# Kernel optimization log

Hardware: AMD Instinct MI355X
Metric: run time of the kernel (lower is better)

The kernel has to match this reference:

```python
import jax, jax.numpy as jnp
import numpy as np

DIM = 256
NUM_HEADS = 8
B = 4
N = 2048
HEAD_DIM = DIM // NUM_HEADS
SCALE = HEAD_DIM ** -0.5
MASK_NEG = -1000.0  # module uses -1000, not -inf


def _block_mask(n):
    # top-left [n/2, n/2] visible, top-right zeroed; bottom [n/2, n] lower-tri with diagonal offset n/2
    half = n // 2
    top = jnp.concatenate([jnp.ones((half, half)), jnp.zeros((half, half))], axis=1)
    bot = jnp.tril(jnp.ones((half, n)), k=half)
    m = jnp.concatenate([top, bot], axis=0)  # [n, n]
    return jnp.where(m != 0, 0.0, MASK_NEG).astype(jnp.float32)


def setup_inputs() -> dict:
    key = jax.random.key(0)
    k1, k2 = jax.random.split(key, 2)
    x = jax.random.normal(k1, (B, N, DIM), dtype=jnp.float32)
    # fused QKV projection params: Linear(dim, 3*dim, bias=True)
    W_qkv = jax.random.normal(k2, (DIM, 3 * DIM), dtype=jnp.float32) * (DIM ** -0.5)
    b_qkv = jnp.zeros((3 * DIM,), dtype=jnp.float32)
    return {"x": x, "W_qkv": W_qkv, "b_qkv": b_qkv}


def reference(x, W_qkv, b_qkv):
    B_, Nn, C = x.shape
    qkv = x @ W_qkv + b_qkv                                   # [B, N, 3C]
    qkv = qkv.reshape(B_, Nn, 3, NUM_HEADS, C // NUM_HEADS)
    qkv = jnp.transpose(qkv, (2, 0, 3, 1, 4))                 # [3, B, H, N, hd]
    q, k, v = qkv[0] * SCALE, qkv[1], qkv[2]
    attn = jnp.einsum('bhqd,bhkd->bhqk', q, k) + _block_mask(Nn)  # [B, H, N, N]
    attn = jax.nn.softmax(attn, axis=-1)
    out = jnp.einsum('bhqk,bhkd->bhqd', attn, v)              # [B, H, N, hd]
    return jnp.transpose(out, (0, 2, 1, 3)).reshape(B_, Nn, C)
```

## Files before the change

kernel.cpp:

```cpp
#include <hip/hip_runtime.h>
#include <cstdint>
#include <cstddef>

typedef unsigned short u16;
typedef unsigned int u32;
typedef __attribute__((ext_vector_type(8))) __bf16 bf16x8;
typedef __attribute__((ext_vector_type(8))) u16 u16x8;
typedef __attribute__((ext_vector_type(4))) float f32x4;

#define N_SEQ   2048
#define HDIM    32
#define QSCALE_LOG2E 0.2550540261150831f

#if __has_builtin(__builtin_amdgcn_exp2f)
#define EXP2(x) __builtin_amdgcn_exp2f(x)
#else
#define EXP2(x) exp2f(x)
#endif

__device__ __forceinline__ u16 f2bf(float f){
  union { float f; u32 i; } v; v.f = f;
  return (u16)((v.i + 0x7FFFu + ((v.i >> 16) & 1u)) >> 16);
}
__device__ __forceinline__ u32 fbits(float f){
  union { float f; u32 i; } v; v.f = f; return v.i;
}
__device__ __forceinline__ u32 pk2bf(float a, float b){
  return ((fbits(a) + 0x8000u) >> 16) | ((fbits(b) + 0x8000u) & 0xFFFF0000u);
}
__device__ __forceinline__ f32x4 mfma_bf16(bf16x8 a, bf16x8 b, f32x4 c){
  return __builtin_amdgcn_mfma_f32_16x16x32_bf16(a, b, c, 0, 0, 0);
}
union U8 { u16x8 u; bf16x8 b; };
union U2 { u32 w[2]; uint64_t q; };

__global__ __launch_bounds__(256) void wt_kernel(const float* __restrict__ W,
                                                 u16* __restrict__ Wt){
  __shared__ u16 T[32][33];
  int t  = threadIdx.x;
  int tx = t & 31, ty = t >> 5;
  int n0 = blockIdx.x * 32;
  int k0 = blockIdx.y * 32;
#pragma unroll
  for (int i = 0; i < 4; ++i){
    int kk = ty + i*8;
    T[kk][tx] = f2bf(W[(k0+kk)*768 + n0 + tx]);
  }
  __syncthreads();
#pragma unroll
  for (int i = 0; i < 4; ++i){
    int nn = ty + i*8;
    Wt[(n0+nn)*256 + k0 + tx] = T[tx][nn];
  }
}

__global__ __launch_bounds__(256) void qkv_kernel(const float* __restrict__ X,
                                                  const u16* __restrict__ Wt,
                                                  const float* __restrict__ bias,
                                                  u16* __restrict__ Q,
                                                  u16* __restrict__ K,
                                                  u16* __restrict__ Vt){
  __shared__ __align__(16) u16 S[64*68];
  int bid = blockIdx.x;
  int xcd = bid & 7;
  int idx = bid >> 3;
  int mt  = 8*(idx & 15) + xcd;
  int nb  = idx >> 4;
  int tid = threadIdx.x;
  int wave = tid >> 6, lane = tid & 63;
  int l16 = lane & 15, quad = lane >> 4;
  int m0 = mt * 64;
  int mw = m0 + wave * 16;
  int n0 = nb * 64;
  const int three = n0 >> 8;

  const float* xr = X + (mw + l16) * 256 + quad * 8;
  U8 af[8];
#pragma unroll
  for (int k = 0; k < 8; ++k){
    f32x4 lo = *(const f32x4*)(xr + k*32);
    f32x4 hi = *(const f32x4*)(xr + k*32 + 4);
    union { u32 w[4]; u16x8 u; } pk;
    pk.w[0] = pk2bf(lo[0], lo[1]);
    pk.w[1] = pk2bf(lo[2], lo[3]);
    pk.w[2] = pk2bf(hi[0], hi[1]);
    pk.w[3] = pk2bf(hi[2], hi[3]);
    af[k].u = pk.u;
  }

  f32x4 acc[4] = {};
#pragma unroll
  for (int k = 0; k < 8; ++k)
#pragma unroll
    for (int s = 0; s < 4; ++s){
      U8 b; b.u = *(const u16x8*)(Wt + (n0 + s*16 + l16)*256 + k*32 + quad*8);
      acc[s] = mfma_bf16(af[k].b, b.b, acc[s]);
    }

  int b_ = m0 >> 11, nseq0 = m0 & 2047;
  if (three == 2){
#pragma unroll
    for (int s = 0; s < 4; ++s){
      int cl = s*16 + l16;
      float bv = bias[n0 + cl];
      int tok = wave*16 + quad*4;
      U2 pk;
      pk.w[0] = pk2bf(acc[s][0] + bv, acc[s][1] + bv);
      pk.w[1] = pk2bf(acc[s][2] + bv, acc[s][3] + bv);
      *(uint64_t*)(&S[cl*68 + tok]) = pk.q;
    }
    __syncthreads();
#pragma unroll
    for (int i = 0; i < 16; ++i){
      int cl = wave*16 + i;
      int c = n0 + cl;
      int h = (c >> 5) & 7, d = c & 31;
      int bh = b_*8 + h;
      int kb = (nseq0 >> 5) + (lane >> 5);
      int kk = lane & 31;
      Vt[((bh*64 + kb)*32 + d)*32 + kk] = S[cl*68 + lane];
    }
  } else {
    float scl = (three == 0) ? QSCALE_LOG2E : 1.0f;
#pragma unroll
    for (int s = 0; s < 4; ++s){
      int cl = s*16 + l16;
      float bv = bias[n0 + cl];
#pragma unroll
      for (int r = 0; r < 4; ++r)
        S[(wave*16 + quad*4 + r)*68 + cl] = f2bf((acc[s][r] + bv) * scl);
    }
    __syncthreads();
    u16* dst = (three == 0) ? Q : K;
#pragma unroll
    for (int j = 0; j < 2; ++j){
      int unit = tid + j*256;
      int tok = unit & 63;
      int rest = unit >> 6;
      int ph = rest >> 2, chunk = rest & 3;
      int h = ((n0 >> 5) + ph) & 7;
      int bh = b_*8 + h;
      u16x8 v = *(const u16x8*)(&S[tok*68 + ph*32 + chunk*8]);
      *(u16x8*)(&dst[(bh*N_SEQ + nseq0 + tok)*HDIM + chunk*8]) = v;
    }
  }
}

__global__ __launch_bounds__(256, 4) void attn_kernel(const u16* __restrict__ Q,
                                                      const u16* __restrict__ Kg,
                                                      const u16* __restrict__ Vt,
                                                      float* __restrict__ out){
  __shared__ __align__(16) u16 smem[4*2*16*72];
  __shared__ float Lbuf[4][32];
  u16  (*Ps)[2][16][72] = (u16 (*)[2][16][72])smem;
  float (*Obuf)[32][36] = (float (*)[32][36])smem;

  int bid = blockIdx.x;
  int bh = (bid & 7)*4 + ((bid >> 3) & 3);
  int g  = bid >> 5;
  int r0 = g * 32;
  int tid = threadIdx.x, wave = tid >> 6, lane = tid & 63;
  int l16 = lane & 15, quad = lane >> 4;

  const u16* Qb = Q  + bh * (N_SEQ*HDIM);
  const u16* Kb = Kg + bh * (N_SEQ*HDIM);
  const u16* Vb = Vt + bh * (64*32*32);

  const int  T       = (r0 < 1024) ? 16 : ((r0 + 31) >> 6) + 1;
  const bool hasMask = (r0 >= 1024);

  U8 qt[2];
  qt[0].u = *(const u16x8*)(Qb + (r0      + l16)*HDIM + quad*8);
  qt[1].u = *(const u16x8*)(Qb + (r0 + 16 + l16)*HDIM + quad*8);

  U8 onesu;
#pragma unroll
  for (int j = 0; j < 8; ++j) onesu.u[j] = 0x3F80;
  bf16x8 ones = onesu.b;

  f32x4 O[2][2] = {};
  f32x4 L[2] = {};

  for (int t = wave; t < T; t += 4){
    int k0 = t * 64;

    U8 kf[4];
#pragma unroll
    for (int s = 0; s < 4; ++s)
      kf[s].u = *(const u16x8*)(Kb + (k0 + s*16 + l16)*HDIM + quad*8);
    U8 vf[2][2];
#pragma unroll
    for (int kc = 0; kc < 2; ++kc)
#pragma unroll
      for (int nd = 0; nd < 2; ++nd)
        vf[kc][nd].u = *(const u16x8*)(Vb + (size_t)(t*2 + kc)*1024 + (nd*16 + l16)*32 + quad*8);

    bool mask = hasMask && (t == T - 1);

#pragma unroll
    for (int qg = 0; qg < 2; ++qg){
      f32x4 ST[4];
#pragma unroll
      for (int s = 0; s < 4; ++s){
        f32x4 z = {};
        ST[s] = mfma_bf16(kf[s].b, qt[qg].b, z);
      }
      u16 (*P)[72] = Ps[wave][qg];
      if (mask){
        int iq = r0 + qg*16 + l16;
#pragma unroll
        for (int s = 0; s < 4; ++s){
          int jb = k0 + s*16 + quad*4;
          float p0 = (jb+0 > iq) ? 0.0f : EXP2(ST[s][0]);
          float p1 = (jb+1 > iq) ? 0.0f : EXP2(ST[s][1]);
          float p2 = (jb+2 > iq) ? 0.0f : EXP2(ST[s][2]);
          float p3 = (jb+3 > iq) ? 0.0f : EXP2(ST[s][3]);
          U2 pk; pk.w[0] = pk2bf(p0, p1); pk.w[1] = pk2bf(p2, p3);
          *(uint64_t*)(&P[l16][s*16 + quad*4]) = pk.q;
        }
      } else {
#pragma unroll
        for (int s = 0; s < 4; ++s){
          U2 pk;
          pk.w[0] = pk2bf(EXP2(ST[s][0]), EXP2(ST[s][1]));
          pk.w[1] = pk2bf(EXP2(ST[s][2]), EXP2(ST[s][3]));
          *(uint64_t*)(&P[l16][s*16 + quad*4]) = pk.q;
        }
      }
    }

#pragma unroll
    for (int qg = 0; qg < 2; ++qg){
      u16 (*P)[72] = Ps[wave][qg];
#pragma unroll
      for (int kc = 0; kc < 2; ++kc){
        U8 pf; pf.u = *(const u16x8*)(&P[l16][kc*32 + quad*8]);
        O[qg][0] = mfma_bf16(pf.b, vf[kc][0].b, O[qg][0]);
        O[qg][1] = mfma_bf16(pf.b, vf[kc][1].b, O[qg][1]);
        L[qg]    = mfma_bf16(pf.b, ones, L[qg]);
      }
    }
  }

  __syncthreads();

#pragma unroll
  for (int qg = 0; qg < 2; ++qg)
#pragma unroll
    for (int r = 0; r < 4; ++r){
      int row = qg*16 + quad*4 + r;
      Obuf[wave][row][l16]      = O[qg][0][r];
      Obuf[wave][row][16 + l16] = O[qg][1][r];
    }
  if (l16 == 0){
#pragma unroll
    for (int qg = 0; qg < 2; ++qg)
#pragma unroll
      for (int r = 0; r < 4; ++r)
        Lbuf[wave][qg*16 + quad*4 + r] = L[qg][r];
  }
  __syncthreads();

  {
    int row = tid >> 3;
    int c4  = (tid & 7) * 4;
    f32x4 a = *(const f32x4*)(&Obuf[0][row][c4]);
    float Ls = Lbuf[0][row];
#pragma unroll
    for (int w = 1; w < 4; ++w){
      f32x4 b = *(const f32x4*)(&Obuf[w][row][c4]);
      a[0] += b[0]; a[1] += b[1]; a[2] += b[2]; a[3] += b[3];
      Ls += Lbuf[w][row];
    }
    float inv = 1.0f / Ls;
    a[0] *= inv; a[1] *= inv; a[2] *= inv; a[3] *= inv;
    int b_ = bh >> 3, h = bh & 7;
    *(f32x4*)(&out[(b_*N_SEQ + r0 + row)*256 + h*32 + c4]) = a;
  }
}

extern "C" void kernel_launch(void* const* d_in, const int* in_sizes, int n_in,
                              void* d_out, int out_size, void* d_ws, size_t ws_size,
                              hipStream_t stream) {
  const float* x    = (const float*)d_in[0];
  const float* W    = (const float*)d_in[1];
  const float* bias = (const float*)d_in[2];
  float* out = (float*)d_out;

  char* ws = (char*)d_ws;
  u16* Wt    = (u16*)(ws);
  u16* Kbuf  = (u16*)(ws + 393216);
  u16* Vtbuf = (u16*)(ws + 393216 + 4194304);
  u16* Qbuf  = (u16*)(ws + 393216 + 2*4194304);

  wt_kernel  <<<dim3(24, 8), 256, 0, stream>>>(W, Wt);
  qkv_kernel <<<dim3(1536),  256, 0, stream>>>(x, Wt, bias, Qbuf, Kbuf, Vtbuf);
  attn_kernel<<<dim3(2048),  256, 0, stream>>>(Qbuf, Kbuf, Vtbuf, out);
}
```

Before: 125.3 us.

## Double attention query tile per block and stage X via LDS with packed W layout

The attention kernel now handles 64 query rows per block instead of 32, with half as many blocks. Each K tile fetched per wave is reused across four query groups, processed in two pairs through the existing P buffer, and the output reduction runs in two passes. The QKV kernel stages the 64x256 X tile into LDS with coalesced loads before building MFMA fragments, and the weight is pre-packed into a fragment-contiguous layout for contiguous B loads. The cost is more registers per attention wave, a larger LDS footprint for the QKV kernel, and fewer blocks to spread across CUs.

```diff
diff --git a/kernel.cpp b/kernel.cpp
--- a/kernel.cpp
+++ b/kernel.cpp
@@ -35,32 +35,27 @@
 union U2 { u32 w[2]; uint64_t q; };
 
 __global__ __launch_bounds__(256) void wt_kernel(const float* __restrict__ W,
-                                                 u16* __restrict__ Wt){
-  __shared__ u16 T[32][33];
+                                                 u16* __restrict__ Wtp){
   int t  = threadIdx.x;
   int tx = t & 31, ty = t >> 5;
   int n0 = blockIdx.x * 32;
   int k0 = blockIdx.y * 32;
 #pragma unroll
   for (int i = 0; i < 4; ++i){
-    int kk = ty + i*8;
-    T[kk][tx] = f2bf(W[(k0+kk)*768 + n0 + tx]);
-  }
-  __syncthreads();
-#pragma unroll
-  for (int i = 0; i < 4; ++i){
-    int nn = ty + i*8;
-    Wt[(n0+nn)*256 + k0 + tx] = T[tx][nn];
+    int k = k0 + ty + i*8;
+    int c = n0 + tx;
+    u16 v = f2bf(W[k*768 + c]);
+    Wtp[((c>>4)*8 + (k>>5))*512 + (c&15)*32 + ((k>>3)&3)*8 + (k&7)] = v;
   }
 }
 
 __global__ __launch_bounds__(256) void qkv_kernel(const float* __restrict__ X,
-                                                  const u16* __restrict__ Wt,
+                                                  const u16* __restrict__ Wtp,
                                                   const float* __restrict__ bias,
                                                   u16* __restrict__ Q,
                                                   u16* __restrict__ K,
                                                   u16* __restrict__ Vt){
-  __shared__ __align__(16) u16 S[64*68];
+  __shared__ __align__(16) u16 SM[64*264];
   int bid = blockIdx.x;
   int xcd = bid & 7;
   int idx = bid >> 3;
@@ -70,30 +65,34 @@
   int wave = tid >> 6, lane = tid & 63;
   int l16 = lane & 15, quad = lane >> 4;
   int m0 = mt * 64;
-  int mw = m0 + wave * 16;
   int n0 = nb * 64;
   const int three = n0 >> 8;
 
-  const float* xr = X + (mw + l16) * 256 + quad * 8;
+  const float* Xblk = X + m0 * 256;
+#pragma unroll
+  for (int i = 0; i < 16; ++i){
+    int e = i*1024 + tid*4;
+    f32x4 v = *(const f32x4*)(Xblk + e);
+    int row = e >> 8, col = e & 255;
+    U2 pk; pk.w[0] = pk2bf(v[0], v[1]); pk.w[1] = pk2bf(v[2], v[3]);
+    *(uint64_t*)(&SM[row*264 + col]) = pk.q;
+  }
+  __syncthreads();
+
+  int mrow = wave*16 + l16;
   U8 af[8];
 #pragma unroll
-  for (int k = 0; k < 8; ++k){
-    f32x4 lo = *(const f32x4*)(xr + k*32);
-    f32x4 hi = *(const f32x4*)(xr + k*32 + 4);
-    union { u32 w[4]; u16x8 u; } pk;
-    pk.w[0] = pk2bf(lo[0], lo[1]);
-    pk.w[1] = pk2bf(lo[2], lo[3]);
-    pk.w[2] = pk2bf(hi[0], hi[1]);
-    pk.w[3] = pk2bf(hi[2], hi[3]);
-    af[k].u = pk.u;
-  }
+  for (int k = 0; k < 8; ++k)
+    af[k].u = *(const u16x8*)(&SM[mrow*264 + k*32 + quad*8]);
+  __syncthreads();
 
   f32x4 acc[4] = {};
 #pragma unroll
   for (int k = 0; k < 8; ++k)
 #pragma unroll
     for (int s = 0; s < 4; ++s){
-      U8 b; b.u = *(const u16x8*)(Wt + (n0 + s*16 + l16)*256 + k*32 + quad*8);
+      U8 b;
+      b.u = *(const u16x8*)(Wtp + (((n0>>4) + s)*8 + k)*512 + l16*32 + quad*8);
       acc[s] = mfma_bf16(af[k].b, b.b, acc[s]);
     }
 
@@ -107,7 +106,7 @@
       U2 pk;
       pk.w[0] = pk2bf(acc[s][0] + bv, acc[s][1] + bv);
       pk.w[1] = pk2bf(acc[s][2] + bv, acc[s][3] + bv);
-      *(uint64_t*)(&S[cl*68 + tok]) = pk.q;
+      *(uint64_t*)(&SM[cl*68 + tok]) = pk.q;
     }
     __syncthreads();
 #pragma unroll
@@ -118,7 +117,7 @@
       int bh = b_*8 + h;
       int kb = (nseq0 >> 5) + (lane >> 5);
       int kk = lane & 31;
-      Vt[((bh*64 + kb)*32 + d)*32 + kk] = S[cl*68 + lane];
+      Vt[((bh*64 + kb)*32 + d)*32 + kk] = SM[cl*68 + lane];
     }
   } else {
     float scl = (three == 0) ? QSCALE_LOG2E : 1.0f;
@@ -128,7 +127,7 @@
       float bv = bias[n0 + cl];
 #pragma unroll
       for (int r = 0; r < 4; ++r)
-        S[(wave*16 + quad*4 + r)*68 + cl] = f2bf((acc[s][r] + bv) * scl);
+        SM[(wave*16 + quad*4 + r)*68 + cl] = f2bf((acc[s][r] + bv) * scl);
     }
     __syncthreads();
     u16* dst = (three == 0) ? Q : K;
@@ -140,7 +139,7 @@
       int ph = rest >> 2, chunk = rest & 3;
       int h = ((n0 >> 5) + ph) & 7;
       int bh = b_*8 + h;
-      u16x8 v = *(const u16x8*)(&S[tok*68 + ph*32 + chunk*8]);
+      u16x8 v = *(const u16x8*)(&SM[tok*68 + ph*32 + chunk*8]);
       *(u16x8*)(&dst[(bh*N_SEQ + nseq0 + tok)*HDIM + chunk*8]) = v;
     }
   }
@@ -158,7 +157,7 @@
   int bid = blockIdx.x;
   int bh = (bid & 7)*4 + ((bid >> 3) & 3);
   int g  = bid >> 5;
-  int r0 = g * 32;
+  int r0 = g * 64;
   int tid = threadIdx.x, wave = tid >> 6, lane = tid & 63;
   int l16 = lane & 15, quad = lane >> 4;
 
@@ -166,116 +165,125 @@
   const u16* Kb = Kg + bh * (N_SEQ*HDIM);
   const u16* Vb = Vt + bh * (64*32*32);
 
-  const int  T       = (r0 < 1024) ? 16 : ((r0 + 31) >> 6) + 1;
+  const int  T       = (r0 < 1024) ? 16 : (g + 1);
   const bool hasMask = (r0 >= 1024);
 
-  U8 qt[2];
-  qt[0].u = *(const u16x8*)(Qb + (r0      + l16)*HDIM + quad*8);
-  qt[1].u = *(const u16x8*)(Qb + (r0 + 16 + l16)*HDIM + quad*8);
+  U8 qt[4];
+#pragma unroll
+  for (int qg = 0; qg < 4; ++qg)
+    qt[qg].u = *(const u16x8*)(Qb + (r0 + qg*16 + l16)*HDIM + quad*8);
 
   U8 onesu;
 #pragma unroll
   for (int j = 0; j < 8; ++j) onesu.u[j] = 0x3F80;
   bf16x8 ones = onesu.b;
 
-  f32x4 O[2][2] = {};
-  f32x4 L[2] = {};
+  f32x4 O[4][2] = {};
+  f32x4 L[4] = {};
 
   for (int t = wave; t < T; t += 4){
     int k0 = t * 64;
-
     U8 kf[4];
 #pragma unroll
     for (int s = 0; s < 4; ++s)
       kf[s].u = *(const u16x8*)(Kb + (k0 + s*16 + l16)*HDIM + quad*8);
-    U8 vf[2][2];
-#pragma unroll
-    for (int kc = 0; kc < 2; ++kc)
-#pragma unroll
-      for (int nd = 0; nd < 2; ++nd)
-        vf[kc][nd].u = *(const u16x8*)(Vb + (size_t)(t*2 + kc)*1024 + (nd*16 + l16)*32 + quad*8);
 
     bool mask = hasMask && (t == T - 1);
 
 #pragma unroll
-    for (int qg = 0; qg < 2; ++qg){
-      f32x4 ST[4];
-#pragma unroll
-      for (int s = 0; s < 4; ++s){
-        f32x4 z = {};
-        ST[s] = mfma_bf16(kf[s].b, qt[qg].b, z);
-      }
-      u16 (*P)[72] = Ps[wave][qg];
-      if (mask){
-        int iq = r0 + qg*16 + l16;
+    for (int pr = 0; pr < 2; ++pr){
+#pragma unroll
+      for (int sub = 0; sub < 2; ++sub){
+        int qg = pr*2 + sub;
+        f32x4 ST[4];
 #pragma unroll
         for (int s = 0; s < 4; ++s){
-          int jb = k0 + s*16 + quad*4;
-          float p0 = (jb+0 > iq) ? 0.0f : EXP2(ST[s][0]);
-          float p1 = (jb+1 > iq) ? 0.0f : EXP2(ST[s][1]);
-          float p2 = (jb+2 > iq) ? 0.0f : EXP2(ST[s][2]);
-          float p3 = (jb+3 > iq) ? 0.0f : EXP2(ST[s][3]);
-          U2 pk; pk.w[0] = pk2bf(p0, p1); pk.w[1] = pk2bf(p2, p3);
-          *(uint64_t*)(&P[l16][s*16 + quad*4]) = pk.q;
+          f32x4 z = {};
+          ST[s] = mfma_bf16(kf[s].b, qt[qg].b, z);
         }
-      } else {
-#pragma unroll
-        for (int s = 0; s < 4; ++s){
-          U2 pk;
-          pk.w[0] = pk2bf(EXP2(ST[s][0]), EXP2(ST[s][1]));
-          pk.w[1] = pk2bf(EXP2(ST[s][2]), EXP2(ST[s][3]));
-          *(uint64_t*)(&P[l16][s*16 + quad*4]) = pk.q;
+        u16 (*P)[72] = Ps[wave][sub];
+        if (mask){
+          int iq = r0 + qg*16 + l16;
+#pragma unroll
+          for (int s = 0; s < 4; ++s){
+            int jb = k0 + s*16 + quad*4;
+            float p0 = (jb+0 > iq) ? 0.0f : EXP2(ST[s][0]);
+            float p1 = (jb+1 > iq) ? 0.0f : EXP2(ST[s][1]);
+            float p2 = (jb+2 > iq) ? 0.0f : EXP2(ST[s][2]);
+            float p3 = (jb+3 > iq) ? 0.0f : EXP2(ST[s][3]);
+            U2 pk; pk.w[0] = pk2bf(p0, p1); pk.w[1] = pk2bf(p2, p3);
+            *(uint64_t*)(&P[l16][s*16 + quad*4]) = pk.q;
+          }
+        } else {
+#pragma unroll
+          for (int s = 0; s < 4; ++s){
+            U2 pk;
+            pk.w[0] = pk2bf(EXP2(ST[s][0]), EXP2(ST[s][1]));
+            pk.w[1] = pk2bf(EXP2(ST[s][2]), EXP2(ST[s][3]));
+            *(uint64_t*)(&P[l16][s*16 + quad*4]) = pk.q;
+          }
         }
       }
-    }
-
-#pragma unroll
-    for (int qg = 0; qg < 2; ++qg){
-      u16 (*P)[72] = Ps[wave][qg];
-#pragma unroll
-      for (int kc = 0; kc < 2; ++kc){
-        U8 pf; pf.u = *(const u16x8*)(&P[l16][kc*32 + quad*8]);
-        O[qg][0] = mfma_bf16(pf.b, vf[kc][0].b, O[qg][0]);
-        O[qg][1] = mfma_bf16(pf.b, vf[kc][1].b, O[qg][1]);
-        L[qg]    = mfma_bf16(pf.b, ones, L[qg]);
+
+      U8 vf[2][2];
+#pragma unroll
+      for (int kc = 0; kc < 2; ++kc)
+#pragma unroll
+        for (int nd = 0; nd < 2; ++nd)
+          vf[kc][nd].u = *(const u16x8*)(Vb + (size_t)(t*2 + kc)*1024 + (nd*16 + l16)*32 + quad*8);
+
+#pragma unroll
+      for (int sub = 0; sub < 2; ++sub){
+        int qg = pr*2 + sub;
+        u16 (*P)[72] = Ps[wave][sub];
+#pragma unroll
+        for (int kc = 0; kc < 2; ++kc){
+          U8 pf; pf.u = *(const u16x8*)(&P[l16][kc*32 + quad*8]);
+          O[qg][0] = mfma_bf16(pf.b, vf[kc][0].b, O[qg][0]);
+          O[qg][1] = mfma_bf16(pf.b, vf[kc][1].b, O[qg][1]);
+          L[qg]    = mfma_bf16(pf.b, ones, L[qg]);
+        }
       }
     }
   }
 
   __syncthreads();
 
-#pragma unroll
-  for (int qg = 0; qg < 2; ++qg)
-#pragma unroll
-    for (int r = 0; r < 4; ++r){
-      int row = qg*16 + quad*4 + r;
-      Obuf[wave][row][l16]      = O[qg][0][r];
-      Obuf[wave][row][16 + l16] = O[qg][1][r];
-    }
-  if (l16 == 0){
-#pragma unroll
-    for (int qg = 0; qg < 2; ++qg)
-#pragma unroll
-      for (int r = 0; r < 4; ++r)
-        Lbuf[wave][qg*16 + quad*4 + r] = L[qg][r];
-  }
-  __syncthreads();
-
-  {
-    int row = tid >> 3;
-    int c4  = (tid & 7) * 4;
-    f32x4 a = *(const f32x4*)(&Obuf[0][row][c4]);
-    float Ls = Lbuf[0][row];
-#pragma unroll
-    for (int w = 1; w < 4; ++w){
-      f32x4 b = *(const f32x4*)(&Obuf[w][row][c4]);
-      a[0] += b[0]; a[1] += b[1]; a[2] += b[2]; a[3] += b[3];
-      Ls += Lbuf[w][row];
-    }
-    float inv = 1.0f / Ls;
-    a[0] *= inv; a[1] *= inv; a[2] *= inv; a[3] *= inv;
-    int b_ = bh >> 3, h = bh & 7;
-    *(f32x4*)(&out[(b_*N_SEQ + r0 + row)*256 + h*32 + c4]) = a;
+  int b_ = bh >> 3, h = bh & 7;
+#pragma unroll
+  for (int pass = 0; pass < 2; ++pass){
+    if (pass) __syncthreads();
+#pragma unroll
+    for (int sub = 0; sub < 2; ++sub){
+      int qg = pass*2 + sub;
+#pragma unroll
+      for (int r = 0; r < 4; ++r){
+        int row = sub*16 + quad*4 + r;
+        Obuf[wave][row][l16]      = O[qg][0][r];
+        Obuf[wave][row][16 + l16] = O[qg][1][r];
+      }
+      if (l16 == 0){
+#pragma unroll
+        for (int r = 0; r < 4; ++r)
+          Lbuf[wave][sub*16 + quad*4 + r] = L[qg][r];
+      }
+    }
+    __syncthreads();
+    {
+      int row = tid >> 3;
+      int c4  = (tid & 7) * 4;
+      f32x4 a = *(const f32x4*)(&Obuf[0][row][c4]);
+      float Ls = Lbuf[0][row];
+#pragma unroll
+      for (int w = 1; w < 4; ++w){
+        f32x4 b = *(const f32x4*)(&Obuf[w][row][c4]);
+        a[0] += b[0]; a[1] += b[1]; a[2] += b[2]; a[3] += b[3];
+        Ls += Lbuf[w][row];
+      }
+      float inv = 1.0f / Ls;
+      a[0] *= inv; a[1] *= inv; a[2] *= inv; a[3] *= inv;
+      *(f32x4*)(&out[(b_*N_SEQ + r0 + pass*32 + row)*256 + h*32 + c4]) = a;
+    }
   }
 }
 
@@ -288,12 +296,12 @@
   float* out = (float*)d_out;
 
   char* ws = (char*)d_ws;
-  u16* Wt    = (u16*)(ws);
+  u16* Wtp   = (u16*)(ws);
   u16* Kbuf  = (u16*)(ws + 393216);
   u16* Vtbuf = (u16*)(ws + 393216 + 4194304);
   u16* Qbuf  = (u16*)(ws + 393216 + 2*4194304);
 
-  wt_kernel  <<<dim3(24, 8), 256, 0, stream>>>(W, Wt);
-  qkv_kernel <<<dim3(1536),  256, 0, stream>>>(x, Wt, bias, Qbuf, Kbuf, Vtbuf);
-  attn_kernel<<<dim3(2048),  256, 0, stream>>>(Qbuf, Kbuf, Vtbuf, out);
-}
+  wt_kernel  <<<dim3(24, 8), 256, 0, stream>>>(W, Wtp);
+  qkv_kernel <<<dim3(1536),  256, 0, stream>>>(x, Wtp, bias, Qbuf, Kbuf, Vtbuf);
+  attn_kernel<<<dim3(1024),  256, 0, stream>>>(Qbuf, Kbuf, Vtbuf, out);
+}
```

After: 120.4 us. -3.9%, faster.
